# Kernel tuning notes

Measured on AMD Instinct MI355X. Metric: run time of the kernel, lower is better.

Reference implementation:

```python
import jax, jax.numpy as jnp
import numpy as np

B, N, D, H, F, K, L, V, E, C = 8, 256, 768, 8, 3072, 128, 8, 32, 1024, 2
HD = D // H
LN_EPS = 1e-3  # keras LayerNormalization default epsilon
GAUSS_A = (2.0 * 3.14159) ** 0.5  # constant from source


def _ln(x, g, b):
    m = jnp.mean(x, axis=-1, keepdims=True)
    v = jnp.mean((x - m) ** 2, axis=-1, keepdims=True)
    return (x - m) * jax.lax.rsqrt(v + LN_EPS) * g + b


def _gelu(x):
    return jax.nn.gelu(x, approximate=False)  # keras 'gelu' is exact


def setup_inputs() -> dict:
    key = jax.random.key(0)
    ks = iter(jax.random.split(key, 40))
    s = 0.02
    inp = {
        'dist': jax.random.uniform(next(ks), (B, N, N), jnp.float32) * 10.0,
        'tok_emb': jax.random.normal(next(ks), (V, D), jnp.float32) * s,
        'gmeans': jax.random.uniform(next(ks), (K,), jnp.float32) * 3.0,
        'gstds': jax.random.uniform(next(ks), (K,), jnp.float32) * 3.0,
        'gmul': jnp.ones((E, 1), jnp.float32),
        'gbias': jnp.zeros((E, 1), jnp.float32),
        'gp1w': jax.random.normal(next(ks), (K, K), jnp.float32) * s,
        'gp1b': jnp.zeros((K,), jnp.float32),
        'gp2w': jax.random.normal(next(ks), (K, H), jnp.float32) * s,
        'gp2b': jnp.zeros((H,), jnp.float32),
        'emb_ln_g': jnp.ones((D,), jnp.float32),
        'emb_ln_b': jnp.zeros((D,), jnp.float32),
        'Wq': jax.random.normal(next(ks), (L, D, D), jnp.float32) * s,
        'bq': jnp.zeros((L, D), jnp.float32),
        'Wo': jax.random.normal(next(ks), (L, D, D), jnp.float32) * s,
        'bo': jnp.zeros((L, D), jnp.float32),
        'ln1g': jnp.ones((L, D), jnp.float32),
        'ln1b': jnp.zeros((L, D), jnp.float32),
        'W1': jax.random.normal(next(ks), (L, D, F), jnp.float32) * s,
        'b1': jnp.zeros((L, F), jnp.float32),
        'W2': jax.random.normal(next(ks), (L, F, D), jnp.float32) * s,
        'b2': jnp.zeros((L, D), jnp.float32),
        'ln2g': jnp.ones((L, D), jnp.float32),
        'ln2b': jnp.zeros((L, D), jnp.float32),
        'fin_ln_g': jnp.ones((D,), jnp.float32),
        'fin_ln_b': jnp.zeros((D,), jnp.float32),
        'cls_w1': jax.random.normal(next(ks), (D, D), jnp.float32) * s,
        'cls_b1': jnp.zeros((D,), jnp.float32),
        'cls_w2': jax.random.normal(next(ks), (D, C), jnp.float32) * s,
        'cls_b2': jnp.zeros((C,), jnp.float32),
        'tokens': jax.random.randint(next(ks), (B, N), 0, V, jnp.int64),
        'edge_type': jax.random.randint(next(ks), (B, N, N), 0, E, jnp.int64),
    }
    return inp


def _forward(dist, tok_emb, gmeans, gstds, gmul, gbias, gp1w, gp1b, gp2w, gp2b,
             emb_ln_g, emb_ln_b, Wq, bq, Wo, bo, ln1g, ln1b, W1, b1, W2, b2,
             ln2g, ln2b, fin_ln_g, fin_ln_b, cls_w1, cls_b1, cls_w2, cls_b2,
             tokens, edge_type):
    # --- Gaussian pairwise bias ---
    mul = gmul[edge_type][..., 0]      # (B,N,N)
    add = gbias[edge_type][..., 0]     # (B,N,N)
    y = mul * dist + add               # (B,N,N)
    std = jnp.abs(gstds) + 1e-5        # (K,)
    g = jnp.exp(-0.5 * ((y[..., None] - gmeans) / std) ** 2) / (GAUSS_A * std)  # (B,N,N,K)
    pb = _gelu(g @ gp1w + gp1b) @ gp2w + gp2b   # (B,N,N,H)
    attn_bias = jnp.transpose(pb, (0, 3, 1, 2))  # (B,H,N,N)

    # --- encoder (pre-LN), NB: wq is shared for q/k/v as in source ---
    x = tok_emb[tokens]                # (B,N,D)
    x = _ln(x, emb_ln_g, emb_ln_b)
    scale = 1.0 / np.sqrt(HD).astype(np.float32)

    def split_heads(t):
        return t.reshape(B, N, H, HD).transpose(0, 2, 1, 3)  # (B,H,N,HD)

    for i in range(L):
        r = x
        h = _ln(x, ln1g[i], ln1b[i])
        q = split_heads((h @ Wq[i] + bq[i]) * scale)
        k = split_heads(h @ Wq[i] + bq[i])
        v = split_heads(h @ Wq[i] + bq[i])
        s = jnp.einsum('bhnd,bhmd->bhnm', q, k) + attn_bias
        p = jax.nn.softmax(s, axis=-1)
        o = jnp.einsum('bhnm,bhmd->bhnd', p, v)
        o = o.transpose(0, 2, 1, 3).reshape(B, N, D) @ Wo[i] + bo[i]
        x = o + r
        r = x
        h = _ln(x, ln2g[i], ln2b[i])
        x = _gelu(h @ W1[i] + b1[i]) @ W2[i] + b2[i] + r
    x = _ln(x, fin_ln_g, fin_ln_b)

    # --- classification head on CLS token ---
    cls = x[:, 0, :]
    return _gelu(cls @ cls_w1 + cls_b1) @ cls_w2 + cls_b2  # (B,C)


def reference(dist, tok_emb, gmeans, gstds, gmul, gbias, gp1w, gp1b, gp2w, gp2b,
              emb_ln_g, emb_ln_b, Wq, bq, Wo, bo, ln1g, ln1b, W1, b1, W2, b2,
              ln2g, ln2b, fin_ln_g, fin_ln_b, cls_w1, cls_b1, cls_w2, cls_b2,
              tokens, edge_type):
    return _forward(dist, tok_emb, gmeans, gstds, gmul, gbias, gp1w, gp1b, gp2w,
                    gp2b, emb_ln_g, emb_ln_b, Wq, bq, Wo, bo, ln1g, ln1b, W1, b1,
                    W2, b2, ln2g, ln2b, fin_ln_g, fin_ln_b, cls_w1, cls_b1,
                    cls_w2, cls_b2, tokens, edge_type)
```

## Files before the change

### kernel.cpp

```cpp
#include <hip/hip_runtime.h>
#include <hip/hip_bf16.h>
#include <math.h>


#define DEV_INLINE __device__ __forceinline__

typedef __attribute__((ext_vector_type(8))) short short8v;
typedef __attribute__((ext_vector_type(4))) short short4v;
typedef __attribute__((ext_vector_type(4))) float f32x4;

DEV_INLINE unsigned short f2bf(float f) {
  unsigned u = __float_as_uint(f);
  return (unsigned short)((u + 0x7fffu + ((u >> 16) & 1u)) >> 16);
}
DEV_INLINE float gelu_f(float v) {
  return 0.5f * v * (1.0f + erff(v * 0.70710678118654752f));
}
DEV_INLINE f32x4 zero4() { f32x4 z; z[0]=0.f; z[1]=0.f; z[2]=0.f; z[3]=0.f; return z; }

__global__ __launch_bounds__(256) void k_cast_t(
    const float* __restrict__ W, unsigned short* __restrict__ Wt, int K, int N)
{
  __shared__ float s[64][68];
  const int tid = threadIdx.x;
  const size_t lay = (size_t)blockIdx.z * K * N;
  const int k0 = blockIdx.x * 64, n0 = blockIdx.y * 64;
  const int r = tid >> 4, c4 = (tid & 15) << 2;
  #pragma unroll
  for (int i = 0; i < 4; ++i)
    *(float4*)&s[r + i * 16][c4] =
        *(const float4*)(W + lay + (size_t)(k0 + r + i * 16) * N + n0 + c4);
  __syncthreads();
  const int n = tid & 63, kc = (tid >> 6) << 4;
  short8v v0, v1;
  #pragma unroll
  for (int j = 0; j < 8; ++j) v0[j] = (short)f2bf(s[kc + j][n]);
  #pragma unroll
  for (int j = 0; j < 8; ++j) v1[j] = (short)f2bf(s[kc + 8 + j][n]);
  unsigned short* dst = Wt + lay + (size_t)(n0 + n) * K + k0 + kc;
  *(short8v*)dst = v0;
  *(short8v*)(dst + 8) = v1;
}

template<int BN, int EPI>
__global__ __launch_bounds__(256) void k_gemm(
    const unsigned short* __restrict__ A, const unsigned short* __restrict__ Bt,
    const float* __restrict__ bias, const float* __restrict__ res,
    void* __restrict__ Cout, int N, int K)
{
  constexpr int NB = BN / 32;
  __shared__ __align__(16) unsigned short As[128 * 64];
  __shared__ __align__(16) unsigned short Bs[BN * 64];
  const int tid = threadIdx.x;
  const int l = tid & 63;
  const int w = tid >> 6, wr = w >> 1, wc = w & 1;
  const int row0 = blockIdx.x * 128, col0 = blockIdx.y * BN;
  const int NT = K >> 6;

  const int rA = tid >> 3;
  const int cs = (((tid & 7) * 16) ^ ((rA & 7) << 4)) >> 1;
  const unsigned short* pa = A + (size_t)(row0 + rA) * K + (tid & 7) * 8;
  const unsigned short* pb = Bt + (size_t)(col0 + rA) * K + (tid & 7) * 8;

  short8v ra[4], rb[NB];
  #pragma unroll
  for (int i = 0; i < 4; ++i) ra[i] = *(const short8v*)(pa + (size_t)i * 32 * K);
  #pragma unroll
  for (int i = 0; i < NB; ++i) rb[i] = *(const short8v*)(pb + (size_t)i * 32 * K);

  f32x4 acc[4][NB];
  #pragma unroll
  for (int mi = 0; mi < 4; ++mi)
    #pragma unroll
    for (int ni = 0; ni < NB; ++ni) acc[mi][ni] = zero4();

  for (int kt = 0; kt < NT; ++kt) {
    #pragma unroll
    for (int i = 0; i < 4; ++i) *(short8v*)&As[(rA + i * 32) * 64 + cs] = ra[i];
    #pragma unroll
    for (int i = 0; i < NB; ++i) *(short8v*)&Bs[(rA + i * 32) * 64 + cs] = rb[i];
    __syncthreads();
    if (kt + 1 < NT) {
      const unsigned short* qa = pa + (size_t)(kt + 1) * 64;
      const unsigned short* qb = pb + (size_t)(kt + 1) * 64;
      #pragma unroll
      for (int i = 0; i < 4; ++i) ra[i] = *(const short8v*)(qa + (size_t)i * 32 * K);
      #pragma unroll
      for (int i = 0; i < NB; ++i) rb[i] = *(const short8v*)(qb + (size_t)i * 32 * K);
    }
    #pragma unroll
    for (int kk = 0; kk < 2; ++kk) {
      short8v af[4], bf_[NB];
      #pragma unroll
      for (int mi = 0; mi < 4; ++mi) {
        int rw = wr * 64 + mi * 16 + (l & 15);
        int kb = (kk * 64 + ((l >> 4) << 4)) ^ ((rw & 7) << 4);
        af[mi] = *(const short8v*)&As[rw * 64 + (kb >> 1)];
      }
      #pragma unroll
      for (int ni = 0; ni < NB; ++ni) {
        int rw = wc * (BN / 2) + ni * 16 + (l & 15);
        int kb = (kk * 64 + ((l >> 4) << 4)) ^ ((rw & 7) << 4);
        bf_[ni] = *(const short8v*)&Bs[rw * 64 + (kb >> 1)];
      }
      #pragma unroll
      for (int mi = 0; mi < 4; ++mi)
        #pragma unroll
        for (int ni = 0; ni < NB; ++ni)
          acc[mi][ni] = __builtin_amdgcn_mfma_f32_16x16x32_bf16(
              af[mi], bf_[ni], acc[mi][ni], 0, 0, 0);
    }
    __syncthreads();
  }

  const int cl = l & 15, rg = (l >> 4) << 2;
  float bv[NB];
  #pragma unroll
  for (int ni = 0; ni < NB; ++ni)
    bv[ni] = bias[col0 + wc * (BN / 2) + ni * 16 + cl];
  #pragma unroll
  for (int mi = 0; mi < 4; ++mi) {
    #pragma unroll
    for (int r = 0; r < 4; ++r) {
      size_t rowg = row0 + wr * 64 + mi * 16 + rg + r;
      #pragma unroll
      for (int ni = 0; ni < NB; ++ni) {
        size_t off = rowg * N + col0 + wc * (BN / 2) + ni * 16 + cl;
        float v = acc[mi][ni][r] + bv[ni];
        if (EPI == 0) ((unsigned short*)Cout)[off] = f2bf(v);
        if (EPI == 1) ((unsigned short*)Cout)[off] = f2bf(gelu_f(v));
        if (EPI == 2) ((float*)Cout)[off] = v + res[off];
      }
    }
  }
}

__global__ __launch_bounds__(256) void k_gauss(
    const float* __restrict__ dist, const int* __restrict__ edge,
    const float* __restrict__ gmul, const float* __restrict__ gbias,
    const float* __restrict__ gmeans, const float* __restrict__ gstds,
    const unsigned short* __restrict__ gp1wt, const float* __restrict__ gp1b,
    const float* __restrict__ gp2w, const float* __restrict__ gp2b,
    float* __restrict__ bias_out)
{
  __shared__ float ys[64];
  __shared__ float mean_s[128], inv_s[128], coef_s[128], b1s[128];
  __shared__ float b2s[8];
  __shared__ __align__(16) unsigned short t1[64 * 128];
  __shared__ __align__(16) unsigned short w2t[16 * 136];
  const int tid = threadIdx.x, l = tid & 63, w = tid >> 6;
  const int pos0 = blockIdx.x * 64;

  if (tid < 128) {
    float sd = fabsf(gstds[tid]) + 1e-5f;
    inv_s[tid] = 1.0f / sd;
    coef_s[tid] = 0.39894250f / sd;
    mean_s[tid] = gmeans[tid];
    b1s[tid] = gp1b[tid];
  }
  if (tid < 8) b2s[tid] = gp2b[tid];
  for (int i = tid; i < 2048; i += 256) {
    int hh = i & 15, k = i >> 4;
    w2t[hh * 136 + k] = (hh < 8) ? f2bf(gp2w[k * 8 + hh]) : (unsigned short)0;
  }
  if (tid < 64) {
    int p = pos0 + tid;
    int et = edge[p];
    ys[tid] = gmul[et] * dist[p] + gbias[et];
  }
  __syncthreads();

  short8v ga[4];
  const float y = ys[w * 16 + (l & 15)];
  #pragma unroll
  for (int ks = 0; ks < 4; ++ks) {
    #pragma unroll
    for (int j = 0; j < 8; ++j) {
      int k = ks * 32 + ((l >> 4) << 3) + j;
      float z = (y - mean_s[k]) * inv_s[k];
      ga[ks][j] = (short)f2bf(__expf(-0.5f * z * z) * coef_s[k]);
    }
  }
  f32x4 acc[8];
  #pragma unroll
  for (int n = 0; n < 8; ++n) {
    acc[n] = zero4();
    const unsigned short* bp = gp1wt + (size_t)(n * 16 + (l & 15)) * 128 + ((l >> 4) << 3);
    #pragma unroll
    for (int ks = 0; ks < 4; ++ks)
      acc[n] = __builtin_amdgcn_mfma_f32_16x16x32_bf16(
          ga[ks], *(const short8v*)(bp + ks * 32), acc[n], 0, 0, 0);
  }
  {
    int rbase = w * 16 + ((l >> 4) << 2);
    #pragma unroll
    for (int n = 0; n < 8; ++n) {
      int col2 = (n * 16 + (l & 15)) * 2;
      float bb = b1s[n * 16 + (l & 15)];
      #pragma unroll
      for (int r = 0; r < 4; ++r) {
        int row = rbase + r;
        int byte = row * 256 + (col2 ^ ((row & 7) << 4));
        t1[byte >> 1] = f2bf(gelu_f(acc[n][r] + bb));
      }
    }
  }
  __syncthreads();
  f32x4 o4 = zero4();
  {
    int row = w * 16 + (l & 15);
    int swz = (row & 7) << 4;
    #pragma unroll
    for (int ks = 0; ks < 4; ++ks) {
      short8v af = *(const short8v*)&t1[(row * 256 + ((ks * 64 + ((l >> 4) << 4)) ^ swz)) >> 1];
      short8v bf_ = *(const short8v*)&w2t[(l & 15) * 136 + ks * 32 + ((l >> 4) << 3)];
      o4 = __builtin_amdgcn_mfma_f32_16x16x32_bf16(af, bf_, o4, 0, 0, 0);
    }
  }
  int hh = l & 15;
  if (hh < 8) {
    int b = pos0 >> 16;
    int ij = (pos0 & 65535) + w * 16 + ((l >> 4) << 2);
    float4 vv;
    vv.x = o4[0] + b2s[hh]; vv.y = o4[1] + b2s[hh];
    vv.z = o4[2] + b2s[hh]; vv.w = o4[3] + b2s[hh];
    *(float4*)(bias_out + ((size_t)((b << 3) + hh) << 16) + ij) = vv;
  }
}

__global__ __launch_bounds__(256) void k_embed_ln(
    const float* __restrict__ emb, const int* __restrict__ tokens,
    const float* __restrict__ g, const float* __restrict__ bp,
    float* __restrict__ out)
{
  __shared__ float red[4], red2[4];
  const int t = threadIdx.x;
  const int row = blockIdx.x;
  const float* xr = emb + (size_t)tokens[row] * 768;
  float v0 = xr[t], v1 = xr[t + 256], v2 = xr[t + 512];
  float s = v0 + v1 + v2;
  #pragma unroll
  for (int o = 32; o; o >>= 1) s += __shfl_down(s, o);
  if ((t & 63) == 0) red[t >> 6] = s;
  __syncthreads();
  float mean = (red[0] + red[1] + red[2] + red[3]) * (1.0f / 768.0f);
  float d0 = v0 - mean, d1 = v1 - mean, d2 = v2 - mean;
  float q = d0 * d0 + d1 * d1 + d2 * d2;
  #pragma unroll
  for (int o = 32; o; o >>= 1) q += __shfl_down(q, o);
  if ((t & 63) == 0) red2[t >> 6] = q;
  __syncthreads();
  float rstd = rsqrtf((red2[0] + red2[1] + red2[2] + red2[3]) * (1.0f / 768.0f) + 1e-3f);
  float* outr = out + (size_t)row * 768;
  outr[t]       = d0 * rstd * g[t]       + bp[t];
  outr[t + 256] = d1 * rstd * g[t + 256] + bp[t + 256];
  outr[t + 512] = d2 * rstd * g[t + 512] + bp[t + 512];
}

__global__ __launch_bounds__(256) void k_ln_bf(
    const float* __restrict__ in, const float* __restrict__ g,
    const float* __restrict__ bp, unsigned short* __restrict__ out)
{
  __shared__ float red[4], red2[4];
  const int t = threadIdx.x;
  const size_t base = (size_t)blockIdx.x * 768;
  const float* xr = in + base;
  float v0 = xr[t], v1 = xr[t + 256], v2 = xr[t + 512];
  float s = v0 + v1 + v2;
  #pragma unroll
  for (int o = 32; o; o >>= 1) s += __shfl_down(s, o);
  if ((t & 63) == 0) red[t >> 6] = s;
  __syncthreads();
  float mean = (red[0] + red[1] + red[2] + red[3]) * (1.0f / 768.0f);
  float d0 = v0 - mean, d1 = v1 - mean, d2 = v2 - mean;
  float q = d0 * d0 + d1 * d1 + d2 * d2;
  #pragma unroll
  for (int o = 32; o; o >>= 1) q += __shfl_down(q, o);
  if ((t & 63) == 0) red2[t >> 6] = q;
  __syncthreads();
  float rstd = rsqrtf((red2[0] + red2[1] + red2[2] + red2[3]) * (1.0f / 768.0f) + 1e-3f);
  unsigned short* outr = out + base;
  outr[t]       = f2bf(d0 * rstd * g[t]       + bp[t]);
  outr[t + 256] = f2bf(d1 * rstd * g[t + 256] + bp[t + 256]);
  outr[t + 512] = f2bf(d2 * rstd * g[t + 512] + bp[t + 512]);
}

__global__ __launch_bounds__(256) void k_transV(
    const unsigned short* __restrict__ P, unsigned short* __restrict__ Vt)
{
  __shared__ unsigned short s[64 * 100];
  const int tid = threadIdx.x;
  const int i0 = blockIdx.x * 64, bh = blockIdx.y, b = bh >> 3, h = bh & 7;
  const unsigned short* Pb = P + ((size_t)b * 256 + i0) * 768 + h * 96;
  #pragma unroll
  for (int i = 0; i < 6; ++i) {
    int o = (tid + i * 256) * 8;
    int row = o / 192, c = o - row * 192;
    *(short4v*)&s[row * 100 + (c >> 1)] =
        *(const short4v*)(Pb + (size_t)row * 768 + (c >> 1));
  }
  __syncthreads();
  #pragma unroll
  for (int i = 0; i < 3; ++i) {
    int u = tid + i * 256;
    int d = u >> 3, tk = (u & 7) << 3;
    short8v v;
    #pragma unroll
    for (int j = 0; j < 8; ++j) v[j] = (short)s[(tk + j) * 100 + d];
    *(short8v*)(Vt + ((size_t)bh * 96 + d) * 256 + i0 + tk) = v;
  }
}

__global__ __launch_bounds__(256) void k_scores_sm(
    const unsigned short* __restrict__ P, const float* __restrict__ bias,
    unsigned short* __restrict__ probs)
{
  __shared__ __align__(16) unsigned short Ks[256 * 96];
  const int tid = threadIdx.x, l = tid & 63, w = tid >> 6;
  const int i0 = blockIdx.x * 64, bh = blockIdx.y, b = bh >> 3, h = bh & 7;
  const unsigned short* Pb = P + (size_t)b * 256 * 768 + h * 96;
  #pragma unroll
  for (int i = 0; i < 12; ++i) {
    int o = i * 4096 + tid * 16;
    int row = o / 192, c = o - row * 192;
    short8v v = *(const short8v*)(Pb + (size_t)row * 768 + (c >> 1));
    *(short8v*)&Ks[row * 96 + ((c ^ ((row & 3) << 4)) >> 1)] = v;
  }
  short8v aq[3];
  const int rq = i0 + w * 16 + (l & 15);
  #pragma unroll
  for (int ks = 0; ks < 3; ++ks)
    aq[ks] = *(const short8v*)(Pb + (size_t)rq * 768 + ks * 32 + ((l >> 4) << 3));
  __syncthreads();

  f32x4 acc[16];
  #pragma unroll
  for (int n = 0; n < 16; ++n) {
    acc[n] = zero4();
    int rk = n * 16 + (l & 15);
    int swz = (rk & 3) << 4;
    #pragma unroll
    for (int ks = 0; ks < 3; ++ks) {
      short8v bq = *(const short8v*)&Ks[rk * 96 + (((ks * 64 + ((l >> 4) << 4)) ^ swz) >> 1)];
      acc[n] = __builtin_amdgcn_mfma_f32_16x16x32_bf16(aq[ks], bq, acc[n], 0, 0, 0);
    }
  }
  const float scale = 0.10206207261596577f;
  const int cl = l & 15;
  const size_t base = ((size_t)bh * 256 + i0 + w * 16 + ((l >> 4) << 2)) * 256 + cl;
  #pragma unroll
  for (int r = 0; r < 4; ++r) {
    size_t rb = base + (size_t)r * 256;
    float m = -1e30f;
    #pragma unroll
    for (int n = 0; n < 16; ++n) {
      float v = acc[n][r] * scale + bias[rb + n * 16];
      acc[n][r] = v;
      m = fmaxf(m, v);
    }
    m = fmaxf(m, __shfl_xor(m, 1)); m = fmaxf(m, __shfl_xor(m, 2));
    m = fmaxf(m, __shfl_xor(m, 4)); m = fmaxf(m, __shfl_xor(m, 8));
    float sum = 0.f;
    #pragma unroll
    for (int n = 0; n < 16; ++n) {
      float e = __expf(acc[n][r] - m);
      acc[n][r] = e;
      sum += e;
    }
    sum += __shfl_xor(sum, 1); sum += __shfl_xor(sum, 2);
    sum += __shfl_xor(sum, 4); sum += __shfl_xor(sum, 8);
    float inv = 1.0f / sum;
    #pragma unroll
    for (int n = 0; n < 16; ++n)
      probs[rb + n * 16] = f2bf(acc[n][r] * inv);
  }
}

__global__ __launch_bounds__(256) void k_pv(
    const unsigned short* __restrict__ probs, const unsigned short* __restrict__ Vt,
    unsigned short* __restrict__ O)
{
  __shared__ __align__(16) unsigned short Vs[96 * 256];
  const int tid = threadIdx.x, l = tid & 63, w = tid >> 6;
  const int i0 = blockIdx.x * 64, bh = blockIdx.y, b = bh >> 3, h = bh & 7;
  const unsigned short* Vb = Vt + (size_t)bh * 96 * 256;
  #pragma unroll
  for (int i = 0; i < 12; ++i) {
    int o = i * 4096 + tid * 16;
    int row = o >> 9, c = o & 511;
    short8v v = *(const short8v*)(Vb + row * 256 + (c >> 1));
    *(short8v*)&Vs[row * 256 + ((c ^ ((row & 7) << 4)) >> 1)] = v;
  }
  short8v pa[8];
  const size_t prow = ((size_t)bh * 256 + i0 + w * 16 + (l & 15)) * 256;
  #pragma unroll
  for (int ks = 0; ks < 8; ++ks)
    pa[ks] = *(const short8v*)(probs + prow + ks * 32 + ((l >> 4) << 3));
  __syncthreads();

  f32x4 acc[6];
  #pragma unroll
  for (int n = 0; n < 6; ++n) {
    acc[n] = zero4();
    int rv = n * 16 + (l & 15);
    int swz = (rv & 7) << 4;
    #pragma unroll
    for (int ks = 0; ks < 8; ++ks) {
      short8v bq = *(const short8v*)&Vs[rv * 256 + (((ks * 64 + ((l >> 4) << 4)) ^ swz) >> 1)];
      acc[n] = __builtin_amdgcn_mfma_f32_16x16x32_bf16(pa[ks], bq, acc[n], 0, 0, 0);
    }
  }
  unsigned short* Ob = O + ((size_t)b * 256 + i0 + w * 16 + ((l >> 4) << 2)) * 768 + h * 96 + (l & 15);
  #pragma unroll
  for (int n = 0; n < 6; ++n)
    #pragma unroll
    for (int r = 0; r < 4; ++r)
      Ob[(size_t)r * 768 + n * 16] = f2bf(acc[n][r]);
}

__global__ __launch_bounds__(256) void k_cls(
    const float* __restrict__ x, const float* __restrict__ fg,
    const float* __restrict__ fb, const float* __restrict__ w1,
    const float* __restrict__ b1, const float* __restrict__ w2,
    const float* __restrict__ b2, float* __restrict__ out)
{
  __shared__ float ln[768];
  __shared__ float t1[768];
  __shared__ float red[8];
  __shared__ float r2[8];
  const int t = threadIdx.x;
  const int b = blockIdx.x;
  const float* xr = x + (size_t)b * 256 * 768;
  float v0 = xr[t], v1 = xr[t + 256], v2 = xr[t + 512];
  float s = v0 + v1 + v2;
  #pragma unroll
  for (int o = 32; o; o >>= 1) s += __shfl_down(s, o);
  if ((t & 63) == 0) red[t >> 6] = s;
  __syncthreads();
  float mean = (red[0] + red[1] + red[2] + red[3]) * (1.0f / 768.0f);
  float d0 = v0 - mean, d1 = v1 - mean, d2 = v2 - mean;
  float q = d0 * d0 + d1 * d1 + d2 * d2;
  #pragma unroll
  for (int o = 32; o; o >>= 1) q += __shfl_down(q, o);
  if ((t & 63) == 0) red[4 + (t >> 6)] = q;
  __syncthreads();
  float rstd = rsqrtf((red[4] + red[5] + red[6] + red[7]) * (1.0f / 768.0f) + 1e-3f);
  ln[t]       = d0 * rstd * fg[t]       + fb[t];
  ln[t + 256] = d1 * rstd * fg[t + 256] + fb[t + 256];
  ln[t + 512] = d2 * rstd * fg[t + 512] + fb[t + 512];
  __syncthreads();
  float a0 = b1[t], a1 = b1[t + 256], a2 = b1[t + 512];
  for (int d = 0; d < 768; ++d) {
    float lv = ln[d];
    a0 = fmaf(lv, w1[d * 768 + t], a0);
    a1 = fmaf(lv, w1[d * 768 + t + 256], a1);
    a2 = fmaf(lv, w1[d * 768 + t + 512], a2);
  }
  t1[t]       = gelu_f(a0);
  t1[t + 256] = gelu_f(a1);
  t1[t + 512] = gelu_f(a2);
  __syncthreads();
  float p0 = 0.f, p1 = 0.f;
  #pragma unroll
  for (int oo = 0; oo < 3; ++oo) {
    int d = t + oo * 256;
    p0 = fmaf(t1[d], w2[d * 2], p0);
    p1 = fmaf(t1[d], w2[d * 2 + 1], p1);
  }
  #pragma unroll
  for (int o = 32; o; o >>= 1) {
    p0 += __shfl_down(p0, o);
    p1 += __shfl_down(p1, o);
  }
  if ((t & 63) == 0) { r2[t >> 6] = p0; r2[4 + (t >> 6)] = p1; }
  __syncthreads();
  if (t == 0) {
    out[b * 2]     = r2[0] + r2[1] + r2[2] + r2[3] + b2[0];
    out[b * 2 + 1] = r2[4] + r2[5] + r2[6] + r2[7] + b2[1];
  }
}

extern "C" void kernel_launch(void* const* d_in, const int* in_sizes, int n_in,
                              void* d_out, int out_size, void* d_ws, size_t ws_size,
                              hipStream_t stream)
{
  const float* dist    = (const float*)d_in[0];
  const float* tok_emb = (const float*)d_in[1];
  const float* gmeans  = (const float*)d_in[2];
  const float* gstds   = (const float*)d_in[3];
  const float* gmul    = (const float*)d_in[4];
  const float* gbias   = (const float*)d_in[5];
  const float* gp1w    = (const float*)d_in[6];
  const float* gp1b    = (const float*)d_in[7];
  const float* gp2w    = (const float*)d_in[8];
  const float* gp2b    = (const float*)d_in[9];
  const float* embg    = (const float*)d_in[10];
  const float* embb    = (const float*)d_in[11];
  const float* Wq      = (const float*)d_in[12];
  const float* bq      = (const float*)d_in[13];
  const float* Wo      = (const float*)d_in[14];
  const float* bo      = (const float*)d_in[15];
  const float* ln1g    = (const float*)d_in[16];
  const float* ln1b    = (const float*)d_in[17];
  const float* W1      = (const float*)d_in[18];
  const float* b1      = (const float*)d_in[19];
  const float* W2      = (const float*)d_in[20];
  const float* b2      = (const float*)d_in[21];
  const float* ln2g    = (const float*)d_in[22];
  const float* ln2b    = (const float*)d_in[23];
  const float* fing    = (const float*)d_in[24];
  const float* finb    = (const float*)d_in[25];
  const float* cw1     = (const float*)d_in[26];
  const float* cb1     = (const float*)d_in[27];
  const float* cw2     = (const float*)d_in[28];
  const float* cb2     = (const float*)d_in[29];
  const int*   tokens  = (const int*)d_in[30];
  const int*   edge    = (const int*)d_in[31];

  float* ws   = (float*)d_ws;
  float* bias = ws;
  float* x    = bias + 4194304;
  unsigned short* hO    = (unsigned short*)(x + 1572864);
  unsigned short* P     = hO + 1572864;
  unsigned short* big   = P + 1572864;
  unsigned short* probs = big;
  unsigned short* Vt    = big + 4194304;
  unsigned short* f1    = big;
  unsigned short* Wqt   = big + 6291456;
  unsigned short* Wot   = Wqt + 4718592;
  unsigned short* W1t   = Wot + 4718592;
  unsigned short* W2t   = W1t + 18874368;
  unsigned short* g1t   = W2t + 18874368;

  k_cast_t<<<dim3(12, 12, 8), 256, 0, stream>>>(Wq, Wqt, 768, 768);
  k_cast_t<<<dim3(12, 12, 8), 256, 0, stream>>>(Wo, Wot, 768, 768);
  k_cast_t<<<dim3(12, 48, 8), 256, 0, stream>>>(W1, W1t, 768, 3072);
  k_cast_t<<<dim3(48, 12, 8), 256, 0, stream>>>(W2, W2t, 3072, 768);
  k_cast_t<<<dim3(2, 2, 1), 256, 0, stream>>>(gp1w, g1t, 128, 128);

  k_gauss<<<8192, 256, 0, stream>>>(dist, edge, gmul, gbias, gmeans, gstds,
                                    g1t, gp1b, gp2w, gp2b, bias);
  k_embed_ln<<<2048, 256, 0, stream>>>(tok_emb, tokens, embg, embb, x);

  for (int l = 0; l < 8; ++l) {
    k_ln_bf<<<2048, 256, 0, stream>>>(x, ln1g + l * 768, ln1b + l * 768, hO);
    k_gemm<64, 0><<<dim3(16, 12), 256, 0, stream>>>(
        hO, Wqt + (size_t)l * 589824, bq + l * 768, nullptr, P, 768, 768);
    k_transV<<<dim3(4, 64), 256, 0, stream>>>(P, Vt);
    k_scores_sm<<<dim3(4, 64), 256, 0, stream>>>(P, bias, probs);
    k_pv<<<dim3(4, 64), 256, 0, stream>>>(probs, Vt, hO);
    k_gemm<64, 2><<<dim3(16, 12), 256, 0, stream>>>(
        hO, Wot + (size_t)l * 589824, bo + l * 768, x, x, 768, 768);
    k_ln_bf<<<2048, 256, 0, stream>>>(x, ln2g + l * 768, ln2b + l * 768, hO);
    k_gemm<128, 1><<<dim3(16, 24), 256, 0, stream>>>(
        hO, W1t + (size_t)l * 2359296, b1 + l * 3072, nullptr, f1, 3072, 768);
    k_gemm<64, 2><<<dim3(16, 12), 256, 0, stream>>>(
        f1, W2t + (size_t)l * 2359296, b2 + l * 768, x, x, 768, 3072);
  }
  k_cls<<<8, 256, 0, stream>>>(x, fing, finb, cw1, cb1, cw2, cb2, (float*)d_out);
}
```

Measured before the change: 1.135 ms.

## Fuse attention kernels, split-K FFN2 with fused residual+LN, direct global-to-LDS GEMM loads

Merges score/softmax and PV into one attention kernel that keeps probabilities in per-wave LDS and normalizes at output, removing the probs round trip through global memory. The GEMM now uses global_load_lds direct copies instead of register staging, but this drops the register double-buffering of the next tile. The FFN2 GEMM is split along K into two partial outputs, and a new fused kernel sums the partials with the residual and computes the next layer's LN1. k_gauss now keeps its staging buffer per wave, removing one block barrier. Both split-K and the loss of prefetch can add latency or traffic.

```diff
diff --git a/kernel.cpp b/kernel.cpp
--- a/kernel.cpp
+++ b/kernel.cpp
@@ -9,6 +9,12 @@
 typedef __attribute__((ext_vector_type(4))) short short4v;
 typedef __attribute__((ext_vector_type(4))) float f32x4;
 
+typedef __attribute__((address_space(1))) const unsigned int GLD_SRC;
+typedef __attribute__((address_space(3))) unsigned int LDS_DST;
+
+DEV_INLINE void gload16(const unsigned short* g, unsigned short* l) {
+  __builtin_amdgcn_global_load_lds((GLD_SRC*)(const void*)g, (LDS_DST*)(void*)l, 16, 0, 0);
+}
 DEV_INLINE unsigned short f2bf(float f) {
   unsigned u = __float_as_uint(f);
   return (unsigned short)((u + 0x7fffu + ((u >> 16) & 1u)) >> 16);
@@ -46,7 +52,7 @@
 __global__ __launch_bounds__(256) void k_gemm(
     const unsigned short* __restrict__ A, const unsigned short* __restrict__ Bt,
     const float* __restrict__ bias, const float* __restrict__ res,
-    void* __restrict__ Cout, int N, int K)
+    void* __restrict__ C0, void* __restrict__ C1, int N, int Kfull, int Klen)
 {
   constexpr int NB = BN / 32;
   __shared__ __align__(16) unsigned short As[128 * 64];
@@ -55,18 +61,20 @@
   const int l = tid & 63;
   const int w = tid >> 6, wr = w >> 1, wc = w & 1;
   const int row0 = blockIdx.x * 128, col0 = blockIdx.y * BN;
-  const int NT = K >> 6;
-
-  const int rA = tid >> 3;
-  const int cs = (((tid & 7) * 16) ^ ((rA & 7) << 4)) >> 1;
-  const unsigned short* pa = A + (size_t)(row0 + rA) * K + (tid & 7) * 8;
-  const unsigned short* pb = Bt + (size_t)(col0 + rA) * K + (tid & 7) * 8;
-
-  short8v ra[4], rb[NB];
-  #pragma unroll
-  for (int i = 0; i < 4; ++i) ra[i] = *(const short8v*)(pa + (size_t)i * 32 * K);
-  #pragma unroll
-  for (int i = 0; i < NB; ++i) rb[i] = *(const short8v*)(pb + (size_t)i * 32 * K);
+  const int z = blockIdx.z;
+  const int Koff = z * Klen;
+  const int NT = Klen >> 6;
+
+  const int lr = l >> 3;
+  const int lc = ((l & 7) ^ lr) << 3;
+  const unsigned short* gA[4];
+  #pragma unroll
+  for (int i = 0; i < 4; ++i)
+    gA[i] = A + (size_t)(row0 + w * 32 + i * 8 + lr) * Kfull + Koff + lc;
+  const unsigned short* gB[NB];
+  #pragma unroll
+  for (int i = 0; i < NB; ++i)
+    gB[i] = Bt + (size_t)(col0 + w * (8 * NB) + i * 8 + lr) * Kfull + Koff + lc;
 
   f32x4 acc[4][NB];
   #pragma unroll
@@ -76,18 +84,12 @@
 
   for (int kt = 0; kt < NT; ++kt) {
     #pragma unroll
-    for (int i = 0; i < 4; ++i) *(short8v*)&As[(rA + i * 32) * 64 + cs] = ra[i];
-    #pragma unroll
-    for (int i = 0; i < NB; ++i) *(short8v*)&Bs[(rA + i * 32) * 64 + cs] = rb[i];
+    for (int i = 0; i < 4; ++i)
+      gload16(gA[i] + kt * 64, &As[(w * 32 + i * 8) * 64]);
+    #pragma unroll
+    for (int i = 0; i < NB; ++i)
+      gload16(gB[i] + kt * 64, &Bs[(w * (8 * NB) + i * 8) * 64]);
     __syncthreads();
-    if (kt + 1 < NT) {
-      const unsigned short* qa = pa + (size_t)(kt + 1) * 64;
-      const unsigned short* qb = pb + (size_t)(kt + 1) * 64;
-      #pragma unroll
-      for (int i = 0; i < 4; ++i) ra[i] = *(const short8v*)(qa + (size_t)i * 32 * K);
-      #pragma unroll
-      for (int i = 0; i < NB; ++i) rb[i] = *(const short8v*)(qb + (size_t)i * 32 * K);
-    }
     #pragma unroll
     for (int kk = 0; kk < 2; ++kk) {
       short8v af[4], bf_[NB];
@@ -114,10 +116,11 @@
   }
 
   const int cl = l & 15, rg = (l >> 4) << 2;
+  void* Cv = (EPI == 3 && z) ? C1 : C0;
   float bv[NB];
   #pragma unroll
   for (int ni = 0; ni < NB; ++ni)
-    bv[ni] = bias[col0 + wc * (BN / 2) + ni * 16 + cl];
+    bv[ni] = (EPI == 3 && z) ? 0.f : bias[col0 + wc * (BN / 2) + ni * 16 + cl];
   #pragma unroll
   for (int mi = 0; mi < 4; ++mi) {
     #pragma unroll
@@ -127,9 +130,10 @@
       for (int ni = 0; ni < NB; ++ni) {
         size_t off = rowg * N + col0 + wc * (BN / 2) + ni * 16 + cl;
         float v = acc[mi][ni][r] + bv[ni];
-        if (EPI == 0) ((unsigned short*)Cout)[off] = f2bf(v);
-        if (EPI == 1) ((unsigned short*)Cout)[off] = f2bf(gelu_f(v));
-        if (EPI == 2) ((float*)Cout)[off] = v + res[off];
+        if (EPI == 0) ((unsigned short*)Cv)[off] = f2bf(v);
+        if (EPI == 1) ((unsigned short*)Cv)[off] = f2bf(gelu_f(v));
+        if (EPI == 2) ((float*)Cv)[off] = v + res[off];
+        if (EPI == 3) ((float*)Cv)[off] = v;
       }
     }
   }
@@ -143,11 +147,10 @@
     const float* __restrict__ gp2w, const float* __restrict__ gp2b,
     float* __restrict__ bias_out)
 {
-  __shared__ float ys[64];
   __shared__ float mean_s[128], inv_s[128], coef_s[128], b1s[128];
   __shared__ float b2s[8];
-  __shared__ __align__(16) unsigned short t1[64 * 128];
   __shared__ __align__(16) unsigned short w2t[16 * 136];
+  __shared__ __align__(16) unsigned short t1[4][2048];
   const int tid = threadIdx.x, l = tid & 63, w = tid >> 6;
   const int pos0 = blockIdx.x * 64;
 
@@ -163,15 +166,13 @@
     int hh = i & 15, k = i >> 4;
     w2t[hh * 136 + k] = (hh < 8) ? f2bf(gp2w[k * 8 + hh]) : (unsigned short)0;
   }
-  if (tid < 64) {
-    int p = pos0 + tid;
-    int et = edge[p];
-    ys[tid] = gmul[et] * dist[p] + gbias[et];
-  }
-  __syncthreads();
+  __syncthreads();
+
+  const int p = pos0 + w * 16 + (l & 15);
+  const int et = edge[p];
+  const float y = gmul[et] * dist[p] + gbias[et];
 
   short8v ga[4];
-  const float y = ys[w * 16 + (l & 15)];
   #pragma unroll
   for (int ks = 0; ks < 4; ++ks) {
     #pragma unroll
@@ -191,33 +192,33 @@
       acc[n] = __builtin_amdgcn_mfma_f32_16x16x32_bf16(
           ga[ks], *(const short8v*)(bp + ks * 32), acc[n], 0, 0, 0);
   }
+  unsigned short* tw = t1[w];
   {
-    int rbase = w * 16 + ((l >> 4) << 2);
+    const int rb = (l >> 4) << 2;
     #pragma unroll
     for (int n = 0; n < 8; ++n) {
       int col2 = (n * 16 + (l & 15)) * 2;
       float bb = b1s[n * 16 + (l & 15)];
       #pragma unroll
       for (int r = 0; r < 4; ++r) {
-        int row = rbase + r;
-        int byte = row * 256 + (col2 ^ ((row & 7) << 4));
-        t1[byte >> 1] = f2bf(gelu_f(acc[n][r] + bb));
+        int row = rb + r;
+        int swz = ((row & 3) << 4) ^ ((row >> 2) << 5);
+        tw[(row * 256 + (col2 ^ swz)) >> 1] = f2bf(gelu_f(acc[n][r] + bb));
       }
     }
   }
-  __syncthreads();
   f32x4 o4 = zero4();
   {
-    int row = w * 16 + (l & 15);
-    int swz = (row & 7) << 4;
+    const int row = l & 15;
+    const int swz = ((row & 3) << 4) ^ ((row >> 2) << 5);
     #pragma unroll
     for (int ks = 0; ks < 4; ++ks) {
-      short8v af = *(const short8v*)&t1[(row * 256 + ((ks * 64 + ((l >> 4) << 4)) ^ swz)) >> 1];
+      short8v af = *(const short8v*)&tw[(row * 256 + ((ks * 64 + ((l >> 4) << 4)) ^ swz)) >> 1];
       short8v bf_ = *(const short8v*)&w2t[(l & 15) * 136 + ks * 32 + ((l >> 4) << 3)];
       o4 = __builtin_amdgcn_mfma_f32_16x16x32_bf16(af, bf_, o4, 0, 0, 0);
     }
   }
-  int hh = l & 15;
+  const int hh = l & 15;
   if (hh < 8) {
     int b = pos0 >> 16;
     int ij = (pos0 & 65535) + w * 16 + ((l >> 4) << 2);
@@ -285,6 +286,41 @@
   outr[t + 512] = f2bf(d2 * rstd * g[t + 512] + bp[t + 512]);
 }
 
+template<int DO_LN>
+__global__ __launch_bounds__(256) void k_fuse(
+    const float* __restrict__ p0, const float* __restrict__ p1,
+    const float* __restrict__ g, const float* __restrict__ bp,
+    float* __restrict__ x, unsigned short* __restrict__ h)
+{
+  __shared__ float red[4], red2[4];
+  const int t = threadIdx.x;
+  const size_t base = (size_t)blockIdx.x * 768;
+  float v0 = p0[base + t]       + p1[base + t]       + x[base + t];
+  float v1 = p0[base + t + 256] + p1[base + t + 256] + x[base + t + 256];
+  float v2 = p0[base + t + 512] + p1[base + t + 512] + x[base + t + 512];
+  x[base + t]       = v0;
+  x[base + t + 256] = v1;
+  x[base + t + 512] = v2;
+  if (DO_LN) {
+    float s = v0 + v1 + v2;
+    #pragma unroll
+    for (int o = 32; o; o >>= 1) s += __shfl_down(s, o);
+    if ((t & 63) == 0) red[t >> 6] = s;
+    __syncthreads();
+    float mean = (red[0] + red[1] + red[2] + red[3]) * (1.0f / 768.0f);
+    float d0 = v0 - mean, d1 = v1 - mean, d2 = v2 - mean;
+    float q = d0 * d0 + d1 * d1 + d2 * d2;
+    #pragma unroll
+    for (int o = 32; o; o >>= 1) q += __shfl_down(q, o);
+    if ((t & 63) == 0) red2[t >> 6] = q;
+    __syncthreads();
+    float rstd = rsqrtf((red2[0] + red2[1] + red2[2] + red2[3]) * (1.0f / 768.0f) + 1e-3f);
+    h[base + t]       = f2bf(d0 * rstd * g[t]       + bp[t]);
+    h[base + t + 256] = f2bf(d1 * rstd * g[t + 256] + bp[t + 256]);
+    h[base + t + 512] = f2bf(d2 * rstd * g[t + 512] + bp[t + 512]);
+  }
+}
+
 __global__ __launch_bounds__(256) void k_transV(
     const unsigned short* __restrict__ P, unsigned short* __restrict__ Vt)
 {
@@ -311,111 +347,84 @@
   }
 }
 
-__global__ __launch_bounds__(256) void k_scores_sm(
-    const unsigned short* __restrict__ P, const float* __restrict__ bias,
-    unsigned short* __restrict__ probs)
-{
-  __shared__ __align__(16) unsigned short Ks[256 * 96];
+__global__ __launch_bounds__(256) void k_attn(
+    const unsigned short* __restrict__ P, const unsigned short* __restrict__ Vt,
+    const float* __restrict__ bias, unsigned short* __restrict__ O)
+{
+  __shared__ __align__(16) unsigned short pl[4][4096];
   const int tid = threadIdx.x, l = tid & 63, w = tid >> 6;
-  const int i0 = blockIdx.x * 64, bh = blockIdx.y, b = bh >> 3, h = bh & 7;
-  const unsigned short* Pb = P + (size_t)b * 256 * 768 + h * 96;
-  #pragma unroll
-  for (int i = 0; i < 12; ++i) {
-    int o = i * 4096 + tid * 16;
-    int row = o / 192, c = o - row * 192;
-    short8v v = *(const short8v*)(Pb + (size_t)row * 768 + (c >> 1));
-    *(short8v*)&Ks[row * 96 + ((c ^ ((row & 3) << 4)) >> 1)] = v;
-  }
+  const int i0 = blockIdx.x << 6, bh = blockIdx.y, b = bh >> 3, hh = bh & 7;
+  const unsigned short* Pb = P + (size_t)b * 196608 + hh * 96;
+
   short8v aq[3];
   const int rq = i0 + w * 16 + (l & 15);
   #pragma unroll
   for (int ks = 0; ks < 3; ++ks)
     aq[ks] = *(const short8v*)(Pb + (size_t)rq * 768 + ks * 32 + ((l >> 4) << 3));
-  __syncthreads();
 
   f32x4 acc[16];
   #pragma unroll
   for (int n = 0; n < 16; ++n) {
     acc[n] = zero4();
-    int rk = n * 16 + (l & 15);
-    int swz = (rk & 3) << 4;
-    #pragma unroll
-    for (int ks = 0; ks < 3; ++ks) {
-      short8v bq = *(const short8v*)&Ks[rk * 96 + (((ks * 64 + ((l >> 4) << 4)) ^ swz) >> 1)];
-      acc[n] = __builtin_amdgcn_mfma_f32_16x16x32_bf16(aq[ks], bq, acc[n], 0, 0, 0);
-    }
-  }
+    const unsigned short* kp = Pb + (size_t)(n * 16 + (l & 15)) * 768 + ((l >> 4) << 3);
+    #pragma unroll
+    for (int ks = 0; ks < 3; ++ks)
+      acc[n] = __builtin_amdgcn_mfma_f32_16x16x32_bf16(
+          aq[ks], *(const short8v*)(kp + ks * 32), acc[n], 0, 0, 0);
+  }
+
   const float scale = 0.10206207261596577f;
-  const int cl = l & 15;
-  const size_t base = ((size_t)bh * 256 + i0 + w * 16 + ((l >> 4) << 2)) * 256 + cl;
+  float inv[4];
+  unsigned short* plw = pl[w];
+  const size_t brow = ((size_t)bh * 256 + i0 + w * 16 + ((l >> 4) << 2)) * 256 + (l & 15);
   #pragma unroll
   for (int r = 0; r < 4; ++r) {
-    size_t rb = base + (size_t)r * 256;
+    const float* bptr = bias + brow + (size_t)r * 256;
     float m = -1e30f;
     #pragma unroll
     for (int n = 0; n < 16; ++n) {
-      float v = acc[n][r] * scale + bias[rb + n * 16];
+      float v = acc[n][r] * scale + bptr[n * 16];
       acc[n][r] = v;
       m = fmaxf(m, v);
     }
     m = fmaxf(m, __shfl_xor(m, 1)); m = fmaxf(m, __shfl_xor(m, 2));
     m = fmaxf(m, __shfl_xor(m, 4)); m = fmaxf(m, __shfl_xor(m, 8));
-    float sum = 0.f;
+    const int rowL = ((l >> 4) << 2) + r;
+    const int swz = ((rowL & 3) << 4) ^ ((rowL >> 2) << 5);
+    const int cb = (l & 15) << 1;
+    float s = 0.f;
     #pragma unroll
     for (int n = 0; n < 16; ++n) {
       float e = __expf(acc[n][r] - m);
-      acc[n][r] = e;
-      sum += e;
-    }
-    sum += __shfl_xor(sum, 1); sum += __shfl_xor(sum, 2);
-    sum += __shfl_xor(sum, 4); sum += __shfl_xor(sum, 8);
-    float inv = 1.0f / sum;
-    #pragma unroll
-    for (int n = 0; n < 16; ++n)
-      probs[rb + n * 16] = f2bf(acc[n][r] * inv);
-  }
-}
-
-__global__ __launch_bounds__(256) void k_pv(
-    const unsigned short* __restrict__ probs, const unsigned short* __restrict__ Vt,
-    unsigned short* __restrict__ O)
-{
-  __shared__ __align__(16) unsigned short Vs[96 * 256];
-  const int tid = threadIdx.x, l = tid & 63, w = tid >> 6;
-  const int i0 = blockIdx.x * 64, bh = blockIdx.y, b = bh >> 3, h = bh & 7;
-  const unsigned short* Vb = Vt + (size_t)bh * 96 * 256;
-  #pragma unroll
-  for (int i = 0; i < 12; ++i) {
-    int o = i * 4096 + tid * 16;
-    int row = o >> 9, c = o & 511;
-    short8v v = *(const short8v*)(Vb + row * 256 + (c >> 1));
-    *(short8v*)&Vs[row * 256 + ((c ^ ((row & 7) << 4)) >> 1)] = v;
-  }
+      s += e;
+      plw[(rowL * 512 + ((cb + (n << 5)) ^ swz)) >> 1] = f2bf(e);
+    }
+    s += __shfl_xor(s, 1); s += __shfl_xor(s, 2);
+    s += __shfl_xor(s, 4); s += __shfl_xor(s, 8);
+    inv[r] = 1.0f / s;
+  }
+
+  const int rowA = l & 15;
+  const int swzA = ((rowA & 3) << 4) ^ ((rowA >> 2) << 5);
   short8v pa[8];
-  const size_t prow = ((size_t)bh * 256 + i0 + w * 16 + (l & 15)) * 256;
   #pragma unroll
   for (int ks = 0; ks < 8; ++ks)
-    pa[ks] = *(const short8v*)(probs + prow + ks * 32 + ((l >> 4) << 3));
-  __syncthreads();
-
-  f32x4 acc[6];
+    pa[ks] = *(const short8v*)&plw[(rowA * 512 + ((ks * 64 + ((l >> 4) << 4)) ^ swzA)) >> 1];
+
+  unsigned short* Ob = O + ((size_t)b * 256 + i0 + w * 16 + ((l >> 4) << 2)) * 768
+                       + hh * 96 + (l & 15);
   #pragma unroll
   for (int n = 0; n < 6; ++n) {
-    acc[n] = zero4();
-    int rv = n * 16 + (l & 15);
-    int swz = (rv & 7) << 4;
-    #pragma unroll
-    for (int ks = 0; ks < 8; ++ks) {
-      short8v bq = *(const short8v*)&Vs[rv * 256 + (((ks * 64 + ((l >> 4) << 4)) ^ swz) >> 1)];
-      acc[n] = __builtin_amdgcn_mfma_f32_16x16x32_bf16(pa[ks], bq, acc[n], 0, 0, 0);
-    }
-  }
-  unsigned short* Ob = O + ((size_t)b * 256 + i0 + w * 16 + ((l >> 4) << 2)) * 768 + h * 96 + (l & 15);
-  #pragma unroll
-  for (int n = 0; n < 6; ++n)
+    f32x4 a2 = zero4();
+    const unsigned short* vb = Vt + ((size_t)bh * 96 + n * 16 + (l & 15)) * 256 + ((l >> 4) << 3);
+    #pragma unroll
+    for (int ks = 0; ks < 8; ++ks)
+      a2 = __builtin_amdgcn_mfma_f32_16x16x32_bf16(
+          pa[ks], *(const short8v*)(vb + ks * 32), a2, 0, 0, 0);
     #pragma unroll
     for (int r = 0; r < 4; ++r)
-      Ob[(size_t)r * 768 + n * 16] = f2bf(acc[n][r]);
+      Ob[(size_t)r * 768 + n * 16] = f2bf(a2[r] * inv[r]);
+  }
 }
 
 __global__ __launch_bounds__(256) void k_cls(
@@ -520,17 +529,17 @@
   float* ws   = (float*)d_ws;
   float* bias = ws;
   float* x    = bias + 4194304;
-  unsigned short* hO    = (unsigned short*)(x + 1572864);
-  unsigned short* P     = hO + 1572864;
-  unsigned short* big   = P + 1572864;
-  unsigned short* probs = big;
-  unsigned short* Vt    = big + 4194304;
-  unsigned short* f1    = big;
-  unsigned short* Wqt   = big + 6291456;
-  unsigned short* Wot   = Wqt + 4718592;
-  unsigned short* W1t   = Wot + 4718592;
-  unsigned short* W2t   = W1t + 18874368;
-  unsigned short* g1t   = W2t + 18874368;
+  float* p0   = x + 1572864;
+  float* p1   = p0 + 1572864;
+  unsigned short* hO  = (unsigned short*)(p1 + 1572864);
+  unsigned short* P   = hO + 1572864;
+  unsigned short* Vt  = P + 1572864;
+  unsigned short* f1  = Vt + 1572864;
+  unsigned short* Wqt = f1 + 6291456;
+  unsigned short* Wot = Wqt + 4718592;
+  unsigned short* W1t = Wot + 4718592;
+  unsigned short* W2t = W1t + 18874368;
+  unsigned short* g1t = W2t + 18874368;
 
   k_cast_t<<<dim3(12, 12, 8), 256, 0, stream>>>(Wq, Wqt, 768, 768);
   k_cast_t<<<dim3(12, 12, 8), 256, 0, stream>>>(Wo, Wot, 768, 768);
@@ -541,21 +550,25 @@
   k_gauss<<<8192, 256, 0, stream>>>(dist, edge, gmul, gbias, gmeans, gstds,
                                     g1t, gp1b, gp2w, gp2b, bias);
   k_embed_ln<<<2048, 256, 0, stream>>>(tok_emb, tokens, embg, embb, x);
+  k_ln_bf<<<2048, 256, 0, stream>>>(x, ln1g, ln1b, hO);
 
   for (int l = 0; l < 8; ++l) {
-    k_ln_bf<<<2048, 256, 0, stream>>>(x, ln1g + l * 768, ln1b + l * 768, hO);
-    k_gemm<64, 0><<<dim3(16, 12), 256, 0, stream>>>(
-        hO, Wqt + (size_t)l * 589824, bq + l * 768, nullptr, P, 768, 768);
+    k_gemm<64, 0><<<dim3(16, 12, 1), 256, 0, stream>>>(
+        hO, Wqt + (size_t)l * 589824, bq + l * 768, nullptr, P, nullptr, 768, 768, 768);
     k_transV<<<dim3(4, 64), 256, 0, stream>>>(P, Vt);
-    k_scores_sm<<<dim3(4, 64), 256, 0, stream>>>(P, bias, probs);
-    k_pv<<<dim3(4, 64), 256, 0, stream>>>(probs, Vt, hO);
-    k_gemm<64, 2><<<dim3(16, 12), 256, 0, stream>>>(
-        hO, Wot + (size_t)l * 589824, bo + l * 768, x, x, 768, 768);
+    k_attn<<<dim3(4, 64), 256, 0, stream>>>(P, Vt, bias, hO);
+    k_gemm<64, 2><<<dim3(16, 12, 1), 256, 0, stream>>>(
+        hO, Wot + (size_t)l * 589824, bo + l * 768, x, x, nullptr, 768, 768, 768);
     k_ln_bf<<<2048, 256, 0, stream>>>(x, ln2g + l * 768, ln2b + l * 768, hO);
-    k_gemm<128, 1><<<dim3(16, 24), 256, 0, stream>>>(
-        hO, W1t + (size_t)l * 2359296, b1 + l * 3072, nullptr, f1, 3072, 768);
-    k_gemm<64, 2><<<dim3(16, 12), 256, 0, stream>>>(
-        f1, W2t + (size_t)l * 2359296, b2 + l * 768, x, x, 768, 3072);
+    k_gemm<128, 1><<<dim3(16, 24, 1), 256, 0, stream>>>(
+        hO, W1t + (size_t)l * 2359296, b1 + l * 3072, nullptr, f1, nullptr, 3072, 768, 768);
+    k_gemm<64, 3><<<dim3(16, 12, 2), 256, 0, stream>>>(
+        f1, W2t + (size_t)l * 2359296, b2 + l * 768, nullptr, p0, p1, 768, 3072, 1536);
+    if (l < 7)
+      k_fuse<1><<<2048, 256, 0, stream>>>(p0, p1, ln1g + (l + 1) * 768,
+                                          ln1b + (l + 1) * 768, x, hO);
+    else
+      k_fuse<0><<<2048, 256, 0, stream>>>(p0, p1, nullptr, nullptr, x, hO);
   }
   k_cls<<<8, 256, 0, stream>>>(x, fing, finb, cw1, cb1, cw2, cb2, (float*)d_out);
 }
```

Result: slower. 1.268 ms (+11.7%).
